# Optimization experiments

Measured on AMD Instinct MI355X. Metric: run time of the kernel, lower is better.

The kernel has to match this reference:

```python
import jax, jax.numpy as jnp
import numpy as np

B, S, D_MODEL, D_K, D_V = 8, 2048, 1024, 512, 512


def setup_inputs() -> dict:
    key = jax.random.key(0)
    ks = jax.random.split(key, 7)
    sq = jax.random.normal(ks[0], (B, S, D_MODEL), dtype=jnp.float32)
    skv = jax.random.normal(ks[1], (B, S, D_MODEL), dtype=jnp.float32)
    q_pad = jax.random.uniform(ks[2], (B, S)) < 0.1
    kv_pad = jax.random.uniform(ks[3], (B, S)) < 0.1
    Wq = jax.random.normal(ks[4], (D_MODEL, D_K), dtype=jnp.float32) * (D_MODEL ** -0.5)
    Wk = jax.random.normal(ks[5], (D_MODEL, D_K), dtype=jnp.float32) * (D_MODEL ** -0.5)
    Wv = jax.random.normal(ks[6], (D_MODEL, D_V), dtype=jnp.float32) * (D_MODEL ** -0.5)
    return {
        "source_query": sq,
        "source_key_value": skv,
        "source_query_padding_mask": q_pad,
        "source_key_value_padding_mask": kv_pad,
        "Wq": Wq,
        "Wk": Wk,
        "Wv": Wv,
    }


def reference(source_query, source_key_value, source_query_padding_mask,
              source_key_value_padding_mask, Wq, Wk, Wv):
    neg_inf = jnp.float32(-jnp.inf)
    q = source_query @ Wq          # [B,Sq,d_k]
    k = source_key_value @ Wk      # [B,Sk,d_k]
    v = source_key_value @ Wv      # [B,Sk,d_v]
    scale = jnp.float32(D_K) ** -0.5
    scores = jnp.einsum("bqd,bkd->bqk", q, k) * scale  # [B,Sq,Sk]
    # query padding mask broadcast along key dim, kv padding mask along query dim
    pad = source_query_padding_mask[:, :, None] | source_key_value_padding_mask[:, None, :]
    scores = jnp.where(pad, neg_inf, scores)
    # causal mask (masked=True): positions above diagonal blocked
    Sq = scores.shape[1]
    causal = jnp.tril(jnp.ones((Sq, Sq), dtype=bool))
    scores = jnp.where(causal[None, :, :], scores, neg_inf)
    attn = jax.nn.softmax(scores, axis=-1)
    # fully-masked rows produce NaN -> zero (matches torch nan masked_fill)
    attn = jnp.where(jnp.isnan(attn), jnp.float32(0.0), attn)
    # dropout p=0.0 (eval): identity
    out = jnp.einsum("bqk,bkv->bqv", attn, v)  # [B,Sq,d_v]
    return out
```

## Files before the change

kernel.cpp:

```cpp
#include <hip/hip_runtime.h>

typedef unsigned short u16;
typedef unsigned int   u32;
typedef __attribute__((ext_vector_type(4))) float  f32x4;
typedef __attribute__((ext_vector_type(8))) __bf16 bf16x8;

#define BATCH 8
#define SEQ   2048
#define DMODEL 1024
#define DK    512
#define DV    512
#define SCALE 0.044194173824159216f

__device__ __forceinline__ u16 f2bf(float f) {
  u32 u = __float_as_uint(f);
  return (u16)((u + 0x7fffu + ((u >> 16) & 1u)) >> 16);
}

__device__ __forceinline__ bool read_mask(const void* p, int idx, int mode) {
  if (mode == 1) return ((const unsigned char*)p)[idx] != 0;
  if (mode == 2) return ((const float*)p)[idx] != 0.0f;
  return ((const int*)p)[idx] != 0;
}

__device__ __forceinline__ void gl_lds16(const u16* g, u16* l) {
  __builtin_amdgcn_global_load_lds(
      (const __attribute__((address_space(1))) u32*)g,
      (__attribute__((address_space(3))) u32*)l, 16, 0, 0);
}

__global__ void detect_mode(const int* __restrict__ qp, int* __restrict__ flag) {
  __shared__ int f;
  if (threadIdx.x == 0) f = 0;
  __syncthreads();
  int local = 0;
  for (int i = threadIdx.x; i < 4096; i += 256) {
    int v = qp[i];
    if (v == 0x3F800000) local |= 2;
    else if (v != 0 && v != 1 && v != -1) local |= 1;
  }
  if (local) atomicOr(&f, local);
  __syncthreads();
  if (threadIdx.x == 0) {
    int m = 0;
    if (f & 2) m = 2; else if (f & 1) m = 1;
    *flag = m;
  }
}

__global__ __launch_bounds__(256) void wt_transpose(const float* __restrict__ W0,
                                                    const float* __restrict__ W1,
                                                    const float* __restrict__ W2,
                                                    u16* __restrict__ dst) {
  const float* W = (blockIdx.z == 0) ? W0 : (blockIdx.z == 1) ? W1 : W2;
  u16* out = dst + (size_t)blockIdx.z * (DK * DMODEL);
  __shared__ float T[32][33];
  int k0 = blockIdx.x * 32, n0 = blockIdx.y * 32;
  int tx = threadIdx.x, ty = threadIdx.y;
#pragma unroll
  for (int i = 0; i < 4; ++i) {
    int r = ty + i * 8;
    T[r][tx] = W[(size_t)(k0 + r) * DK + n0 + tx];
  }
  __syncthreads();
#pragma unroll
  for (int i = 0; i < 4; ++i) {
    int r = ty + i * 8;
    out[(size_t)(n0 + r) * DMODEL + k0 + tx] = f2bf(T[tx][r]);
  }
}

__global__ __launch_bounds__(256) void convert_bf16(const float* __restrict__ src,
                                                    u16* __restrict__ dst) {
  int i = (blockIdx.x * 256 + threadIdx.x) * 8;
  f32x4 a = *(const f32x4*)(src + i);
  f32x4 b = *(const f32x4*)(src + i + 4);
  uint4 o;
  o.x = (u32)f2bf(a[0]) | ((u32)f2bf(a[1]) << 16);
  o.y = (u32)f2bf(a[2]) | ((u32)f2bf(a[3]) << 16);
  o.z = (u32)f2bf(b[0]) | ((u32)f2bf(b[1]) << 16);
  o.w = (u32)f2bf(b[2]) | ((u32)f2bf(b[3]) << 16);
  *(uint4*)(dst + i) = o;
}

__global__ __launch_bounds__(256, 3) void proj_gemm(const u16* __restrict__ A,
                                                    const u16* __restrict__ Wt_base,
                                                    int z0, u16* __restrict__ dst0,
                                                    u16* __restrict__ dst1) {
  int z = z0 + blockIdx.z;
  const u16* Wt = Wt_base + (size_t)z * (DK * DMODEL);
  u16* dst = (z == 2) ? dst1 : dst0;
  int n0 = blockIdx.x * 128, m0 = blockIdx.y * 128;

  __shared__ __align__(16) u16 As[128 * 64];
  __shared__ __align__(16) u16 Bs[128 * 64];

  int tid = threadIdx.x, lane = tid & 63, w = tid >> 6;
  int wm = w & 1, wn = w >> 1;
  int l15 = lane & 15, lg = lane >> 4;
  int r3 = lane >> 3, c7 = lane & 7;
  int csw = c7 ^ r3;

  f32x4 acc[4][4];
#pragma unroll
  for (int m = 0; m < 4; ++m)
#pragma unroll
    for (int n = 0; n < 4; ++n) acc[m][n] = (f32x4)0.0f;

  for (int k0 = 0; k0 < DMODEL; k0 += 64) {
    __syncthreads();
#pragma unroll
    for (int u = 0; u < 4; ++u) {
      int t = w * 4 + u;
      gl_lds16(A  + (size_t)(m0 + t * 8 + r3) * DMODEL + k0 + csw * 8, &As[t * 512]);
      gl_lds16(Wt + (size_t)(n0 + t * 8 + r3) * DMODEL + k0 + csw * 8, &Bs[t * 512]);
    }
    __syncthreads();
#pragma unroll
    for (int ks = 0; ks < 2; ++ks) {
      bf16x8 af[4], bfv[4];
#pragma unroll
      for (int m = 0; m < 4; ++m) {
        int row = wm * 64 + m * 16 + l15;
        af[m] = *(const bf16x8*)&As[row * 64 + (((ks * 4 + lg) ^ (l15 & 7)) * 8)];
      }
#pragma unroll
      for (int n = 0; n < 4; ++n) {
        int row = wn * 64 + n * 16 + l15;
        bfv[n] = *(const bf16x8*)&Bs[row * 64 + (((ks * 4 + lg) ^ (l15 & 7)) * 8)];
      }
#pragma unroll
      for (int m = 0; m < 4; ++m)
#pragma unroll
        for (int n = 0; n < 4; ++n)
          acc[m][n] = __builtin_amdgcn_mfma_f32_16x16x32_bf16(af[m], bfv[n], acc[m][n], 0, 0, 0);
    }
  }

  if (z != 2) {
#pragma unroll
    for (int m = 0; m < 4; ++m) {
      int rowb = m0 + wm * 64 + m * 16;
#pragma unroll
      for (int n = 0; n < 4; ++n) {
        int col = n0 + wn * 64 + n * 16 + l15;
        size_t base = (size_t)(rowb >> 4) * 8192 + (size_t)(col >> 5) * 512 + (col & 31);
#pragma unroll
        for (int r = 0; r < 4; ++r)
          dst[base + (lg * 4 + r) * 32] = f2bf(acc[m][n][r]);
      }
    }
  } else {
#pragma unroll
    for (int m = 0; m < 4; ++m) {
      int row0 = m0 + wm * 64 + m * 16 + lg * 4;
      int b = row0 >> 11, s0 = row0 & 2047;
#pragma unroll
      for (int n = 0; n < 4; ++n) {
        int dv = n0 + wn * 64 + n * 16 + l15;
        size_t off = (size_t)b * (SEQ * DV) + (size_t)(dv >> 4) * 32768 +
                     (size_t)(s0 >> 5) * 512 + (dv & 15) * 32 + (s0 & 31);
        u16 tmp[4] __attribute__((aligned(8)));
#pragma unroll
        for (int r = 0; r < 4; ++r) tmp[r] = f2bf(acc[m][n][r]);
        *(uint2*)&dst[off] = *(const uint2*)tmp;
      }
    }
  }
}

__global__ __launch_bounds__(256, 2) void attn_kernel(
    const u16* __restrict__ Qf, const u16* __restrict__ Kf,
    const u16* __restrict__ Vf, const void* __restrict__ qpad,
    const void* __restrict__ kvpad, const int* __restrict__ flag,
    float* __restrict__ out) {
  __shared__ __align__(16) u16 Pbuf[32 * 72];
  __shared__ float partm[32 * 2];
  __shared__ float ald[32];
  __shared__ float partl[32 * 2];

  int tid = threadIdx.x;
  int lane = tid & 63, w = tid >> 6;
  int l15 = lane & 15, lg = lane >> 4;
  int wk = w & 1;
  int m  = w >> 1;
  int bi = blockIdx.x;
  int j = bi & 63, b = bi >> 6;
  int qt = (j & 1) ? (63 - (j >> 1)) : (j >> 1);
  int q0 = qt * 32;
  int mode = *flag;
  int lanoff = l15 * 32 + lg * 8;

  const u16* Qb = Qf + (size_t)b * (SEQ * DK);
  const u16* Kb = Kf + (size_t)b * (SEQ * DK);
  const u16* Vb = Vf + (size_t)b * (SEQ * DV);

  bf16x8 qf[16];
  {
    const u16* qp = Qb + (size_t)(qt * 2 + m) * 8192 + lanoff;
#pragma unroll
    for (int ks = 0; ks < 16; ++ks) qf[ks] = *(const bf16x8*)(qp + ks * 512);
  }

  f32x4 o[2][8];
#pragma unroll
  for (int m2 = 0; m2 < 2; ++m2)
#pragma unroll
    for (int n = 0; n < 8; ++n) o[m2][n] = (f32x4)0.0f;

  float mo[4], lsum[4];
#pragma unroll
  for (int r = 0; r < 4; ++r) { mo[r] = -1e38f; lsum[r] = 0.0f; }

  int nkt = (q0 + 95) >> 6;

  for (int kt = 0; kt < nkt; ++kt) {
    int k0 = kt * 64;

    f32x4 s0 = (f32x4)0.0f, s1 = (f32x4)0.0f;
    {
      const u16* kp0 = Kb + (size_t)((k0 >> 4) + wk * 2) * 8192 + lanoff;
      const u16* kp1 = kp0 + 8192;
#pragma unroll
      for (int ks = 0; ks < 16; ++ks) {
        bf16x8 b0 = *(const bf16x8*)(kp0 + ks * 512);
        bf16x8 b1 = *(const bf16x8*)(kp1 + ks * 512);
        s0 = __builtin_amdgcn_mfma_f32_16x16x32_bf16(qf[ks], b0, s0, 0, 0, 0);
        s1 = __builtin_amdgcn_mfma_f32_16x16x32_bf16(qf[ks], b1, s1, 0, 0, 0);
      }
    }

    float sv[2][4];
#pragma unroll
    for (int kg = 0; kg < 2; ++kg) {
      int key = k0 + wk * 32 + kg * 16 + l15;
      bool kvm = read_mask(kvpad, b * SEQ + key, mode);
#pragma unroll
      for (int r = 0; r < 4; ++r) {
        int qrow = q0 + m * 16 + lg * 4 + r;
        float x = (kg == 0 ? s0[r] : s1[r]) * SCALE;
        sv[kg][r] = (kvm || key > qrow) ? -__builtin_inff() : x;
      }
    }

    float wmax[4];
#pragma unroll
    for (int r = 0; r < 4; ++r) wmax[r] = fmaxf(sv[0][r], sv[1][r]);
#pragma unroll
    for (int d = 1; d < 16; d <<= 1)
#pragma unroll
      for (int r = 0; r < 4; ++r) wmax[r] = fmaxf(wmax[r], __shfl_xor(wmax[r], d));
    if (l15 == 0) {
#pragma unroll
      for (int r = 0; r < 4; ++r) partm[(m * 16 + lg * 4 + r) * 2 + wk] = wmax[r];
    }
    __syncthreads();

    float al[4], ws[4];
#pragma unroll
    for (int r = 0; r < 4; ++r) {
      int row = m * 16 + lg * 4 + r;
      float tm = fmaxf(partm[row * 2], partm[row * 2 + 1]);
      float mn = fmaxf(mo[r], fmaxf(tm, -1e38f));
      al[r] = __expf(mo[r] - mn);
      mo[r] = mn;
      float p0 = __expf(sv[0][r] - mn);
      float p1 = __expf(sv[1][r] - mn);
      Pbuf[row * 72 + wk * 32 + l15] = f2bf(p0);
      Pbuf[row * 72 + wk * 32 + 16 + l15] = f2bf(p1);
      ws[r] = p0 + p1;
    }
#pragma unroll
    for (int d = 1; d < 16; d <<= 1)
#pragma unroll
      for (int r = 0; r < 4; ++r) ws[r] += __shfl_xor(ws[r], d);
#pragma unroll
    for (int r = 0; r < 4; ++r) lsum[r] = lsum[r] * al[r] + ws[r];
    if (wk == 0 && l15 == 0) {
#pragma unroll
      for (int r = 0; r < 4; ++r) ald[m * 16 + lg * 4 + r] = al[r];
    }
    __syncthreads();

    float ar[2][4];
#pragma unroll
    for (int m2 = 0; m2 < 2; ++m2)
#pragma unroll
      for (int r = 0; r < 4; ++r) ar[m2][r] = ald[m2 * 16 + lg * 4 + r];
#pragma unroll
    for (int m2 = 0; m2 < 2; ++m2)
#pragma unroll
      for (int n = 0; n < 8; ++n)
#pragma unroll
        for (int r = 0; r < 4; ++r) o[m2][n][r] *= ar[m2][r];

    {
      const u16* vpb = Vb + (size_t)(w * 8) * 32768 + (size_t)(k0 >> 5) * 512 + lanoff;
#pragma unroll
      for (int ks = 0; ks < 2; ++ks) {
        bf16x8 pa0 = *(const bf16x8*)&Pbuf[(l15) * 72 + ks * 32 + lg * 8];
        bf16x8 pa1 = *(const bf16x8*)&Pbuf[(16 + l15) * 72 + ks * 32 + lg * 8];
#pragma unroll
        for (int n = 0; n < 4; ++n) {
          bf16x8 bv0 = *(const bf16x8*)(vpb + (size_t)(n * 2) * 32768 + ks * 512);
          bf16x8 bv1 = *(const bf16x8*)(vpb + (size_t)(n * 2 + 1) * 32768 + ks * 512);
          o[0][n * 2]     = __builtin_amdgcn_mfma_f32_16x16x32_bf16(pa0, bv0, o[0][n * 2], 0, 0, 0);
          o[1][n * 2]     = __builtin_amdgcn_mfma_f32_16x16x32_bf16(pa1, bv0, o[1][n * 2], 0, 0, 0);
          o[0][n * 2 + 1] = __builtin_amdgcn_mfma_f32_16x16x32_bf16(pa0, bv1, o[0][n * 2 + 1], 0, 0, 0);
          o[1][n * 2 + 1] = __builtin_amdgcn_mfma_f32_16x16x32_bf16(pa1, bv1, o[1][n * 2 + 1], 0, 0, 0);
        }
      }
    }
  }

  if (l15 == 0) {
#pragma unroll
    for (int r = 0; r < 4; ++r) partl[(m * 16 + lg * 4 + r) * 2 + wk] = lsum[r];
  }
  __syncthreads();
  {
    float f[2][4];
#pragma unroll
    for (int m2 = 0; m2 < 2; ++m2)
#pragma unroll
      for (int r = 0; r < 4; ++r) {
        int row = m2 * 16 + lg * 4 + r;
        float l = partl[row * 2] + partl[row * 2 + 1];
        bool qp = read_mask(qpad, b * SEQ + q0 + row, mode);
        f[m2][r] = (l > 0.0f && !qp) ? 1.0f / l : 0.0f;
      }
#pragma unroll
    for (int m2 = 0; m2 < 2; ++m2)
#pragma unroll
      for (int n = 0; n < 8; ++n) {
        int dv = w * 128 + n * 16 + l15;
#pragma unroll
        for (int r = 0; r < 4; ++r) {
          int row = m2 * 16 + lg * 4 + r;
          out[(size_t)(b * SEQ + q0 + row) * DV + dv] = o[m2][n][r] * f[m2][r];
        }
      }
  }
}

extern "C" void kernel_launch(void* const* d_in, const int* in_sizes, int n_in,
                              void* d_out, int out_size, void* d_ws, size_t ws_size,
                              hipStream_t stream) {
  const float* sq  = (const float*)d_in[0];
  const float* skv = (const float*)d_in[1];
  const void* qp   = d_in[2];
  const void* kvp  = d_in[3];
  const float* Wq  = (const float*)d_in[4];
  const float* Wk  = (const float*)d_in[5];
  const float* Wv  = (const float*)d_in[6];
  char* ws = (char*)d_ws;

  u16* Abf = (u16*)ws;
  u16* Qf  = (u16*)(ws + 33554432);
  u16* Kf  = (u16*)(ws + 50331648);
  u16* Vf  = (u16*)(ws + 67108864);
  u16* Wt  = (u16*)(ws + 83886080);
  int* flag = (int*)(ws + 87031808);

  wt_transpose<<<dim3(32, 16, 3), dim3(32, 8, 1), 0, stream>>>(Wq, Wk, Wv, Wt);
  detect_mode<<<1, 256, 0, stream>>>((const int*)qp, flag);

  convert_bf16<<<8192, 256, 0, stream>>>(sq, Abf);
  proj_gemm<<<dim3(4, 128, 1), dim3(256), 0, stream>>>(Abf, Wt, 0, Qf, Qf);

  convert_bf16<<<8192, 256, 0, stream>>>(skv, Abf);
  proj_gemm<<<dim3(4, 128, 2), dim3(256), 0, stream>>>(Abf, Wt, 1, Kf, Vf);

  attn_kernel<<<dim3(512), dim3(256), 0, stream>>>(Qf, Kf, Vf, qp, kvp, flag,
                                                   (float*)d_out);
}
```

Baseline: 471.9 us.

## Enlarge attention tiles to 64 queries by 128 keys with Q staged in LDS

After: 592.6 us. +25.6%, slower.

```diff
diff --git a/kernel.cpp b/kernel.cpp
--- a/kernel.cpp
+++ b/kernel.cpp
@@ -169,25 +169,24 @@
   }
 }
 
-__global__ __launch_bounds__(256, 2) void attn_kernel(
+#define KTILE 128
+#define PSTRIDE 136
+__global__ __launch_bounds__(256, 1) void attn_kernel(
     const u16* __restrict__ Qf, const u16* __restrict__ Kf,
     const u16* __restrict__ Vf, const void* __restrict__ qpad,
     const void* __restrict__ kvpad, const int* __restrict__ flag,
     float* __restrict__ out) {
-  __shared__ __align__(16) u16 Pbuf[32 * 72];
-  __shared__ float partm[32 * 2];
-  __shared__ float ald[32];
-  __shared__ float partl[32 * 2];
+  __shared__ __align__(16) u16 Qs[2 * 8192];
+  __shared__ __align__(16) u16 Pbuf[64 * PSTRIDE];
+  __shared__ __align__(16) float partm[64 * 4];
+  __shared__ __align__(16) float partl[64 * 4];
 
   int tid = threadIdx.x;
   int lane = tid & 63, w = tid >> 6;
   int l15 = lane & 15, lg = lane >> 4;
-  int wk = w & 1;
-  int m  = w >> 1;
   int bi = blockIdx.x;
-  int j = bi & 63, b = bi >> 6;
-  int qt = (j & 1) ? (63 - (j >> 1)) : (j >> 1);
-  int q0 = qt * 32;
+  int b = bi & 7, qt = bi >> 3;
+  int q0 = qt * 64;
   int mode = *flag;
   int lanoff = l15 * 32 + lg * 8;
 
@@ -195,149 +194,179 @@
   const u16* Kb = Kf + (size_t)b * (SEQ * DK);
   const u16* Vb = Vf + (size_t)b * (SEQ * DV);
 
-  bf16x8 qf[16];
-  {
-    const u16* qp = Qb + (size_t)(qt * 2 + m) * 8192 + lanoff;
-#pragma unroll
-    for (int ks = 0; ks < 16; ++ks) qf[ks] = *(const bf16x8*)(qp + ks * 512);
-  }
-
-  f32x4 o[2][8];
-#pragma unroll
-  for (int m2 = 0; m2 < 2; ++m2)
-#pragma unroll
-    for (int n = 0; n < 8; ++n) o[m2][n] = (f32x4)0.0f;
-
-  float mo[4], lsum[4];
-#pragma unroll
-  for (int r = 0; r < 4; ++r) { mo[r] = -1e38f; lsum[r] = 0.0f; }
-
-  int nkt = (q0 + 95) >> 6;
+#pragma unroll
+  for (int i = 0; i < 8; ++i) {
+    int t = w * 8 + i;
+    gl_lds16(Qb + (size_t)(qt * 4 + (t >> 4)) * 8192 + (size_t)(t & 15) * 512 + lane * 8,
+             &Qs[t * 512]);
+  }
+  bf16x8 qreg[2][16];
+#pragma unroll
+  for (int mm = 0; mm < 2; ++mm) {
+    const u16* qp = Qb + (size_t)(qt * 4 + 2 + mm) * 8192 + lanoff;
+#pragma unroll
+    for (int ks = 0; ks < 16; ++ks) qreg[mm][ks] = *(const bf16x8*)(qp + ks * 512);
+  }
+  __syncthreads();
+
+  f32x4 o[4][8];
+#pragma unroll
+  for (int m = 0; m < 4; ++m)
+#pragma unroll
+    for (int g = 0; g < 8; ++g) o[m][g] = (f32x4)0.0f;
+
+  float mo[4][4], lsum[4][4];
+#pragma unroll
+  for (int m = 0; m < 4; ++m)
+#pragma unroll
+    for (int r = 0; r < 4; ++r) { mo[m][r] = -1e38f; lsum[m][r] = 0.0f; }
+
+  int nkt = (q0 + 191) >> 7;
 
   for (int kt = 0; kt < nkt; ++kt) {
-    int k0 = kt * 64;
-
-    f32x4 s0 = (f32x4)0.0f, s1 = (f32x4)0.0f;
+    int k0 = kt * KTILE;
+    int kg0 = (k0 >> 4) + w * 2;
+
+    f32x4 s[4][2];
+#pragma unroll
+    for (int m = 0; m < 4; ++m) { s[m][0] = (f32x4)0.0f; s[m][1] = (f32x4)0.0f; }
     {
-      const u16* kp0 = Kb + (size_t)((k0 >> 4) + wk * 2) * 8192 + lanoff;
+      const u16* kp0 = Kb + (size_t)kg0 * 8192 + lanoff;
       const u16* kp1 = kp0 + 8192;
 #pragma unroll
       for (int ks = 0; ks < 16; ++ks) {
-        bf16x8 b0 = *(const bf16x8*)(kp0 + ks * 512);
-        bf16x8 b1 = *(const bf16x8*)(kp1 + ks * 512);
-        s0 = __builtin_amdgcn_mfma_f32_16x16x32_bf16(qf[ks], b0, s0, 0, 0, 0);
-        s1 = __builtin_amdgcn_mfma_f32_16x16x32_bf16(qf[ks], b1, s1, 0, 0, 0);
-      }
-    }
-
-    float sv[2][4];
-#pragma unroll
-    for (int kg = 0; kg < 2; ++kg) {
-      int key = k0 + wk * 32 + kg * 16 + l15;
-      bool kvm = read_mask(kvpad, b * SEQ + key, mode);
+        bf16x8 bk0 = *(const bf16x8*)(kp0 + ks * 512);
+        bf16x8 bk1 = *(const bf16x8*)(kp1 + ks * 512);
+        bf16x8 a0 = *(const bf16x8*)&Qs[ks * 512 + lanoff];
+        bf16x8 a1 = *(const bf16x8*)&Qs[8192 + ks * 512 + lanoff];
+        s[0][0] = __builtin_amdgcn_mfma_f32_16x16x32_bf16(a0, bk0, s[0][0], 0, 0, 0);
+        s[0][1] = __builtin_amdgcn_mfma_f32_16x16x32_bf16(a0, bk1, s[0][1], 0, 0, 0);
+        s[1][0] = __builtin_amdgcn_mfma_f32_16x16x32_bf16(a1, bk0, s[1][0], 0, 0, 0);
+        s[1][1] = __builtin_amdgcn_mfma_f32_16x16x32_bf16(a1, bk1, s[1][1], 0, 0, 0);
+        s[2][0] = __builtin_amdgcn_mfma_f32_16x16x32_bf16(qreg[0][ks], bk0, s[2][0], 0, 0, 0);
+        s[2][1] = __builtin_amdgcn_mfma_f32_16x16x32_bf16(qreg[0][ks], bk1, s[2][1], 0, 0, 0);
+        s[3][0] = __builtin_amdgcn_mfma_f32_16x16x32_bf16(qreg[1][ks], bk0, s[3][0], 0, 0, 0);
+        s[3][1] = __builtin_amdgcn_mfma_f32_16x16x32_bf16(qreg[1][ks], bk1, s[3][1], 0, 0, 0);
+      }
+    }
+
+    int key0 = k0 + w * 32 + l15;
+    bool kvm0 = read_mask(kvpad, b * SEQ + key0, mode);
+    bool kvm1 = read_mask(kvpad, b * SEQ + key0 + 16, mode);
+    float sv[4][2][4];
+#pragma unroll
+    for (int m = 0; m < 4; ++m)
 #pragma unroll
       for (int r = 0; r < 4; ++r) {
         int qrow = q0 + m * 16 + lg * 4 + r;
-        float x = (kg == 0 ? s0[r] : s1[r]) * SCALE;
-        sv[kg][r] = (kvm || key > qrow) ? -__builtin_inff() : x;
-      }
-    }
-
-    float wmax[4];
-#pragma unroll
-    for (int r = 0; r < 4; ++r) wmax[r] = fmaxf(sv[0][r], sv[1][r]);
+        float x0 = s[m][0][r] * SCALE;
+        float x1 = s[m][1][r] * SCALE;
+        sv[m][0][r] = (kvm0 || key0 > qrow) ? -__builtin_inff() : x0;
+        sv[m][1][r] = (kvm1 || key0 + 16 > qrow) ? -__builtin_inff() : x1;
+      }
+
+    float wmax[4][4];
+#pragma unroll
+    for (int m = 0; m < 4; ++m)
+#pragma unroll
+      for (int r = 0; r < 4; ++r) wmax[m][r] = fmaxf(sv[m][0][r], sv[m][1][r]);
 #pragma unroll
     for (int d = 1; d < 16; d <<= 1)
 #pragma unroll
-      for (int r = 0; r < 4; ++r) wmax[r] = fmaxf(wmax[r], __shfl_xor(wmax[r], d));
+      for (int m = 0; m < 4; ++m)
+#pragma unroll
+        for (int r = 0; r < 4; ++r)
+          wmax[m][r] = fmaxf(wmax[m][r], __shfl_xor(wmax[m][r], d));
     if (l15 == 0) {
 #pragma unroll
-      for (int r = 0; r < 4; ++r) partm[(m * 16 + lg * 4 + r) * 2 + wk] = wmax[r];
+      for (int m = 0; m < 4; ++m)
+#pragma unroll
+        for (int r = 0; r < 4; ++r) partm[(m * 16 + lg * 4 + r) * 4 + w] = wmax[m][r];
     }
     __syncthreads();
 
-    float al[4], ws[4];
-#pragma unroll
-    for (int r = 0; r < 4; ++r) {
-      int row = m * 16 + lg * 4 + r;
-      float tm = fmaxf(partm[row * 2], partm[row * 2 + 1]);
-      float mn = fmaxf(mo[r], fmaxf(tm, -1e38f));
-      al[r] = __expf(mo[r] - mn);
-      mo[r] = mn;
-      float p0 = __expf(sv[0][r] - mn);
-      float p1 = __expf(sv[1][r] - mn);
-      Pbuf[row * 72 + wk * 32 + l15] = f2bf(p0);
-      Pbuf[row * 72 + wk * 32 + 16 + l15] = f2bf(p1);
-      ws[r] = p0 + p1;
-    }
+    float al[4][4], ws[4][4];
+#pragma unroll
+    for (int m = 0; m < 4; ++m)
+#pragma unroll
+      for (int r = 0; r < 4; ++r) {
+        int row = m * 16 + lg * 4 + r;
+        f32x4 pm = *(const f32x4*)&partm[row * 4];
+        float tm = fmaxf(fmaxf(pm[0], pm[1]), fmaxf(pm[2], pm[3]));
+        float mn = fmaxf(mo[m][r], fmaxf(tm, -1e38f));
+        al[m][r] = __expf(mo[m][r] - mn);
+        mo[m][r] = mn;
+        float p0 = __expf(sv[m][0][r] - mn);
+        float p1 = __expf(sv[m][1][r] - mn);
+        Pbuf[row * PSTRIDE + w * 32 + l15] = f2bf(p0);
+        Pbuf[row * PSTRIDE + w * 32 + 16 + l15] = f2bf(p1);
+        ws[m][r] = p0 + p1;
+      }
 #pragma unroll
     for (int d = 1; d < 16; d <<= 1)
 #pragma unroll
-      for (int r = 0; r < 4; ++r) ws[r] += __shfl_xor(ws[r], d);
-#pragma unroll
-    for (int r = 0; r < 4; ++r) lsum[r] = lsum[r] * al[r] + ws[r];
-    if (wk == 0 && l15 == 0) {
-#pragma unroll
-      for (int r = 0; r < 4; ++r) ald[m * 16 + lg * 4 + r] = al[r];
-    }
+      for (int m = 0; m < 4; ++m)
+#pragma unroll
+        for (int r = 0; r < 4; ++r) ws[m][r] += __shfl_xor(ws[m][r], d);
+#pragma unroll
+    for (int m = 0; m < 4; ++m)
+#pragma unroll
+      for (int r = 0; r < 4; ++r) lsum[m][r] = lsum[m][r] * al[m][r] + ws[m][r];
+
+#pragma unroll
+    for (int m = 0; m < 4; ++m)
+#pragma unroll
+      for (int g = 0; g < 8; ++g)
+#pragma unroll
+        for (int r = 0; r < 4; ++r) o[m][g][r] *= al[m][r];
+
     __syncthreads();
 
-    float ar[2][4];
-#pragma unroll
-    for (int m2 = 0; m2 < 2; ++m2)
-#pragma unroll
-      for (int r = 0; r < 4; ++r) ar[m2][r] = ald[m2 * 16 + lg * 4 + r];
-#pragma unroll
-    for (int m2 = 0; m2 < 2; ++m2)
-#pragma unroll
-      for (int n = 0; n < 8; ++n)
-#pragma unroll
-        for (int r = 0; r < 4; ++r) o[m2][n][r] *= ar[m2][r];
-
-    {
-      const u16* vpb = Vb + (size_t)(w * 8) * 32768 + (size_t)(k0 >> 5) * 512 + lanoff;
-#pragma unroll
-      for (int ks = 0; ks < 2; ++ks) {
-        bf16x8 pa0 = *(const bf16x8*)&Pbuf[(l15) * 72 + ks * 32 + lg * 8];
-        bf16x8 pa1 = *(const bf16x8*)&Pbuf[(16 + l15) * 72 + ks * 32 + lg * 8];
-#pragma unroll
-        for (int n = 0; n < 4; ++n) {
-          bf16x8 bv0 = *(const bf16x8*)(vpb + (size_t)(n * 2) * 32768 + ks * 512);
-          bf16x8 bv1 = *(const bf16x8*)(vpb + (size_t)(n * 2 + 1) * 32768 + ks * 512);
-          o[0][n * 2]     = __builtin_amdgcn_mfma_f32_16x16x32_bf16(pa0, bv0, o[0][n * 2], 0, 0, 0);
-          o[1][n * 2]     = __builtin_amdgcn_mfma_f32_16x16x32_bf16(pa1, bv0, o[1][n * 2], 0, 0, 0);
-          o[0][n * 2 + 1] = __builtin_amdgcn_mfma_f32_16x16x32_bf16(pa0, bv1, o[0][n * 2 + 1], 0, 0, 0);
-          o[1][n * 2 + 1] = __builtin_amdgcn_mfma_f32_16x16x32_bf16(pa1, bv1, o[1][n * 2 + 1], 0, 0, 0);
-        }
+#pragma unroll
+    for (int ks2 = 0; ks2 < 4; ++ks2) {
+      bf16x8 pa[4];
+#pragma unroll
+      for (int m = 0; m < 4; ++m)
+        pa[m] = *(const bf16x8*)&Pbuf[(m * 16 + l15) * PSTRIDE + ks2 * 32 + lg * 8];
+      const u16* vp = Vb + (size_t)(w * 8) * 32768 + (size_t)(kt * 4 + ks2) * 512 + lanoff;
+#pragma unroll
+      for (int g = 0; g < 8; ++g) {
+        bf16x8 bv = *(const bf16x8*)(vp + (size_t)g * 32768);
+#pragma unroll
+        for (int m = 0; m < 4; ++m)
+          o[m][g] = __builtin_amdgcn_mfma_f32_16x16x32_bf16(pa[m], bv, o[m][g], 0, 0, 0);
       }
     }
   }
 
   if (l15 == 0) {
 #pragma unroll
-    for (int r = 0; r < 4; ++r) partl[(m * 16 + lg * 4 + r) * 2 + wk] = lsum[r];
+    for (int m = 0; m < 4; ++m)
+#pragma unroll
+      for (int r = 0; r < 4; ++r) partl[(m * 16 + lg * 4 + r) * 4 + w] = lsum[m][r];
   }
   __syncthreads();
   {
-    float f[2][4];
-#pragma unroll
-    for (int m2 = 0; m2 < 2; ++m2)
+    float f[4][4];
+#pragma unroll
+    for (int m = 0; m < 4; ++m)
 #pragma unroll
       for (int r = 0; r < 4; ++r) {
-        int row = m2 * 16 + lg * 4 + r;
-        float l = partl[row * 2] + partl[row * 2 + 1];
+        int row = m * 16 + lg * 4 + r;
+        f32x4 pl = *(const f32x4*)&partl[row * 4];
+        float l = pl[0] + pl[1] + pl[2] + pl[3];
         bool qp = read_mask(qpad, b * SEQ + q0 + row, mode);
-        f[m2][r] = (l > 0.0f && !qp) ? 1.0f / l : 0.0f;
-      }
-#pragma unroll
-    for (int m2 = 0; m2 < 2; ++m2)
-#pragma unroll
-      for (int n = 0; n < 8; ++n) {
-        int dv = w * 128 + n * 16 + l15;
+        f[m][r] = (l > 0.0f && !qp) ? 1.0f / l : 0.0f;
+      }
+#pragma unroll
+    for (int m = 0; m < 4; ++m)
+#pragma unroll
+      for (int g = 0; g < 8; ++g) {
+        int dv = w * 128 + g * 16 + l15;
 #pragma unroll
         for (int r = 0; r < 4; ++r) {
-          int row = m2 * 16 + lg * 4 + r;
-          out[(size_t)(b * SEQ + q0 + row) * DV + dv] = o[m2][n][r] * f[m2][r];
+          int row = m * 16 + lg * 4 + r;
+          out[(size_t)(b * SEQ + q0 + row) * DV + dv] = o[m][g][r] * f[m][r];
         }
       }
   }
@@ -371,6 +400,6 @@
   convert_bf16<<<8192, 256, 0, stream>>>(skv, Abf);
   proj_gemm<<<dim3(4, 128, 2), dim3(256), 0, stream>>>(Abf, Wt, 1, Kf, Vf);
 
-  attn_kernel<<<dim3(512), dim3(256), 0, stream>>>(Qf, Kf, Vf, qp, kvp, flag,
+  attn_kernel<<<dim3(256), dim3(256), 0, stream>>>(Qf, Kf, Vf, qp, kvp, flag,
                                                    (float*)d_out);
 }
```

## Restructure attention into 16-row tiles with register-resident softmax, no LDS or barriers

Applied to the files above, without the earlier changes.

Result: slower. 706.3 us (+49.7%).

```diff
diff --git a/kernel.cpp b/kernel.cpp
--- a/kernel.cpp
+++ b/kernel.cpp
@@ -159,7 +159,7 @@
       for (int n = 0; n < 4; ++n) {
         int dv = n0 + wn * 64 + n * 16 + l15;
         size_t off = (size_t)b * (SEQ * DV) + (size_t)(dv >> 4) * 32768 +
-                     (size_t)(s0 >> 5) * 512 + (dv & 15) * 32 + (s0 & 31);
+                     (size_t)(s0 >> 5) * 512 + (dv & 15) * 32 + lg * 8 + (m & 1) * 4;
         u16 tmp[4] __attribute__((aligned(8)));
 #pragma unroll
         for (int r = 0; r < 4; ++r) tmp[r] = f2bf(acc[m][n][r]);
@@ -169,177 +169,125 @@
   }
 }
 
-__global__ __launch_bounds__(256, 2) void attn_kernel(
+__global__ __launch_bounds__(128, 2) void attn_kernel(
     const u16* __restrict__ Qf, const u16* __restrict__ Kf,
     const u16* __restrict__ Vf, const void* __restrict__ qpad,
     const void* __restrict__ kvpad, const int* __restrict__ flag,
     float* __restrict__ out) {
-  __shared__ __align__(16) u16 Pbuf[32 * 72];
-  __shared__ float partm[32 * 2];
-  __shared__ float ald[32];
-  __shared__ float partl[32 * 2];
-
   int tid = threadIdx.x;
-  int lane = tid & 63, w = tid >> 6;
+  int lane = tid & 63;
+  int dvh = tid >> 6;
   int l15 = lane & 15, lg = lane >> 4;
-  int wk = w & 1;
-  int m  = w >> 1;
   int bi = blockIdx.x;
-  int j = bi & 63, b = bi >> 6;
-  int qt = (j & 1) ? (63 - (j >> 1)) : (j >> 1);
-  int q0 = qt * 32;
+  int b = bi & 7;
+  int qt = 127 - (bi >> 3);
+  int q0 = qt * 16;
   int mode = *flag;
   int lanoff = l15 * 32 + lg * 8;
+  int q = q0 + l15;
 
   const u16* Qb = Qf + (size_t)b * (SEQ * DK);
   const u16* Kb = Kf + (size_t)b * (SEQ * DK);
-  const u16* Vb = Vf + (size_t)b * (SEQ * DV);
+  const u16* Vb = Vf + (size_t)b * (SEQ * DV) + (size_t)(dvh * 16) * 32768;
 
   bf16x8 qf[16];
   {
-    const u16* qp = Qb + (size_t)(qt * 2 + m) * 8192 + lanoff;
+    const u16* qp = Qb + (size_t)qt * 8192 + lanoff;
 #pragma unroll
     for (int ks = 0; ks < 16; ++ks) qf[ks] = *(const bf16x8*)(qp + ks * 512);
   }
 
-  f32x4 o[2][8];
-#pragma unroll
-  for (int m2 = 0; m2 < 2; ++m2)
-#pragma unroll
-    for (int n = 0; n < 8; ++n) o[m2][n] = (f32x4)0.0f;
-
-  float mo[4], lsum[4];
-#pragma unroll
-  for (int r = 0; r < 4; ++r) { mo[r] = -1e38f; lsum[r] = 0.0f; }
-
-  int nkt = (q0 + 95) >> 6;
+  f32x4 o[16];
+#pragma unroll
+  for (int g = 0; g < 16; ++g) o[g] = (f32x4)0.0f;
+
+  float mo = -1e38f, lsum = 0.0f;
+  int nkt = (q0 + 47) >> 5;
 
   for (int kt = 0; kt < nkt; ++kt) {
-    int k0 = kt * 64;
+    int k0 = kt * 32;
 
     f32x4 s0 = (f32x4)0.0f, s1 = (f32x4)0.0f;
     {
-      const u16* kp0 = Kb + (size_t)((k0 >> 4) + wk * 2) * 8192 + lanoff;
-      const u16* kp1 = kp0 + 8192;
+      const u16* kp = Kb + (size_t)(k0 >> 4) * 8192 + lanoff;
 #pragma unroll
       for (int ks = 0; ks < 16; ++ks) {
-        bf16x8 b0 = *(const bf16x8*)(kp0 + ks * 512);
-        bf16x8 b1 = *(const bf16x8*)(kp1 + ks * 512);
-        s0 = __builtin_amdgcn_mfma_f32_16x16x32_bf16(qf[ks], b0, s0, 0, 0, 0);
-        s1 = __builtin_amdgcn_mfma_f32_16x16x32_bf16(qf[ks], b1, s1, 0, 0, 0);
-      }
-    }
-
-    float sv[2][4];
-#pragma unroll
-    for (int kg = 0; kg < 2; ++kg) {
-      int key = k0 + wk * 32 + kg * 16 + l15;
-      bool kvm = read_mask(kvpad, b * SEQ + key, mode);
+        bf16x8 a0 = *(const bf16x8*)(kp + ks * 512);
+        bf16x8 a1 = *(const bf16x8*)(kp + 8192 + ks * 512);
+        s0 = __builtin_amdgcn_mfma_f32_16x16x32_bf16(a0, qf[ks], s0, 0, 0, 0);
+        s1 = __builtin_amdgcn_mfma_f32_16x16x32_bf16(a1, qf[ks], s1, 0, 0, 0);
+      }
+    }
+
+    float sv0[4], sv1[4];
+#pragma unroll
+    for (int r = 0; r < 4; ++r) {
+      int key0 = k0 + lg * 4 + r;
+      bool msk0 = read_mask(kvpad, b * SEQ + key0, mode) || (key0 > q);
+      bool msk1 = read_mask(kvpad, b * SEQ + key0 + 16, mode) || (key0 + 16 > q);
+      sv0[r] = msk0 ? -__builtin_inff() : s0[r] * SCALE;
+      sv1[r] = msk1 ? -__builtin_inff() : s1[r] * SCALE;
+    }
+
+    float tmax = fmaxf(fmaxf(fmaxf(sv0[0], sv0[1]), fmaxf(sv0[2], sv0[3])),
+                       fmaxf(fmaxf(sv1[0], sv1[1]), fmaxf(sv1[2], sv1[3])));
+    tmax = fmaxf(tmax, __shfl_xor(tmax, 16));
+    tmax = fmaxf(tmax, __shfl_xor(tmax, 32));
+
+    float mn = fmaxf(mo, fmaxf(tmax, -1e38f));
+    float al = __expf(mo - mn);
+    mo = mn;
+
+    float p0[4], p1[4];
+    float psum = 0.0f;
+#pragma unroll
+    for (int r = 0; r < 4; ++r) {
+      p0[r] = __expf(sv0[r] - mn);
+      p1[r] = __expf(sv1[r] - mn);
+      psum += p0[r] + p1[r];
+    }
+    psum += __shfl_xor(psum, 16);
+    psum += __shfl_xor(psum, 32);
+    lsum = lsum * al + psum;
+
+    u16 pk[8] __attribute__((aligned(16)));
+#pragma unroll
+    for (int r = 0; r < 4; ++r) { pk[r] = f2bf(p0[r]); pk[4 + r] = f2bf(p1[r]); }
+    bf16x8 pa = *(const bf16x8*)pk;
+
+    float alr[4];
+#pragma unroll
+    for (int r = 0; r < 4; ++r) alr[r] = __shfl(al, lg * 4 + r);
+#pragma unroll
+    for (int g = 0; g < 16; ++g)
+#pragma unroll
+      for (int r = 0; r < 4; ++r) o[g][r] *= alr[r];
+
+    {
+      const u16* vp = Vb + (size_t)kt * 512 + lanoff;
+#pragma unroll
+      for (int g = 0; g < 16; ++g) {
+        bf16x8 bv = *(const bf16x8*)(vp + (size_t)g * 32768);
+        o[g] = __builtin_amdgcn_mfma_f32_16x16x32_bf16(pa, bv, o[g], 0, 0, 0);
+      }
+    }
+  }
+
+  {
+    bool qpm = read_mask(qpad, b * SEQ + q, mode);
+    float linv = (lsum > 0.0f && !qpm) ? 1.0f / lsum : 0.0f;
+    float lr[4];
+#pragma unroll
+    for (int r = 0; r < 4; ++r) lr[r] = __shfl(linv, lg * 4 + r);
+#pragma unroll
+    for (int g = 0; g < 16; ++g) {
+      int dv = dvh * 256 + g * 16 + l15;
 #pragma unroll
       for (int r = 0; r < 4; ++r) {
-        int qrow = q0 + m * 16 + lg * 4 + r;
-        float x = (kg == 0 ? s0[r] : s1[r]) * SCALE;
-        sv[kg][r] = (kvm || key > qrow) ? -__builtin_inff() : x;
-      }
-    }
-
-    float wmax[4];
-#pragma unroll
-    for (int r = 0; r < 4; ++r) wmax[r] = fmaxf(sv[0][r], sv[1][r]);
-#pragma unroll
-    for (int d = 1; d < 16; d <<= 1)
-#pragma unroll
-      for (int r = 0; r < 4; ++r) wmax[r] = fmaxf(wmax[r], __shfl_xor(wmax[r], d));
-    if (l15 == 0) {
-#pragma unroll
-      for (int r = 0; r < 4; ++r) partm[(m * 16 + lg * 4 + r) * 2 + wk] = wmax[r];
-    }
-    __syncthreads();
-
-    float al[4], ws[4];
-#pragma unroll
-    for (int r = 0; r < 4; ++r) {
-      int row = m * 16 + lg * 4 + r;
-      float tm = fmaxf(partm[row * 2], partm[row * 2 + 1]);
-      float mn = fmaxf(mo[r], fmaxf(tm, -1e38f));
-      al[r] = __expf(mo[r] - mn);
-      mo[r] = mn;
-      float p0 = __expf(sv[0][r] - mn);
-      float p1 = __expf(sv[1][r] - mn);
-      Pbuf[row * 72 + wk * 32 + l15] = f2bf(p0);
-      Pbuf[row * 72 + wk * 32 + 16 + l15] = f2bf(p1);
-      ws[r] = p0 + p1;
-    }
-#pragma unroll
-    for (int d = 1; d < 16; d <<= 1)
-#pragma unroll
-      for (int r = 0; r < 4; ++r) ws[r] += __shfl_xor(ws[r], d);
-#pragma unroll
-    for (int r = 0; r < 4; ++r) lsum[r] = lsum[r] * al[r] + ws[r];
-    if (wk == 0 && l15 == 0) {
-#pragma unroll
-      for (int r = 0; r < 4; ++r) ald[m * 16 + lg * 4 + r] = al[r];
-    }
-    __syncthreads();
-
-    float ar[2][4];
-#pragma unroll
-    for (int m2 = 0; m2 < 2; ++m2)
-#pragma unroll
-      for (int r = 0; r < 4; ++r) ar[m2][r] = ald[m2 * 16 + lg * 4 + r];
-#pragma unroll
-    for (int m2 = 0; m2 < 2; ++m2)
-#pragma unroll
-      for (int n = 0; n < 8; ++n)
-#pragma unroll
-        for (int r = 0; r < 4; ++r) o[m2][n][r] *= ar[m2][r];
-
-    {
-      const u16* vpb = Vb + (size_t)(w * 8) * 32768 + (size_t)(k0 >> 5) * 512 + lanoff;
-#pragma unroll
-      for (int ks = 0; ks < 2; ++ks) {
-        bf16x8 pa0 = *(const bf16x8*)&Pbuf[(l15) * 72 + ks * 32 + lg * 8];
-        bf16x8 pa1 = *(const bf16x8*)&Pbuf[(16 + l15) * 72 + ks * 32 + lg * 8];
-#pragma unroll
-        for (int n = 0; n < 4; ++n) {
-          bf16x8 bv0 = *(const bf16x8*)(vpb + (size_t)(n * 2) * 32768 + ks * 512);
-          bf16x8 bv1 = *(const bf16x8*)(vpb + (size_t)(n * 2 + 1) * 32768 + ks * 512);
-          o[0][n * 2]     = __builtin_amdgcn_mfma_f32_16x16x32_bf16(pa0, bv0, o[0][n * 2], 0, 0, 0);
-          o[1][n * 2]     = __builtin_amdgcn_mfma_f32_16x16x32_bf16(pa1, bv0, o[1][n * 2], 0, 0, 0);
-          o[0][n * 2 + 1] = __builtin_amdgcn_mfma_f32_16x16x32_bf16(pa0, bv1, o[0][n * 2 + 1], 0, 0, 0);
-          o[1][n * 2 + 1] = __builtin_amdgcn_mfma_f32_16x16x32_bf16(pa1, bv1, o[1][n * 2 + 1], 0, 0, 0);
-        }
-      }
-    }
-  }
-
-  if (l15 == 0) {
-#pragma unroll
-    for (int r = 0; r < 4; ++r) partl[(m * 16 + lg * 4 + r) * 2 + wk] = lsum[r];
-  }
-  __syncthreads();
-  {
-    float f[2][4];
-#pragma unroll
-    for (int m2 = 0; m2 < 2; ++m2)
-#pragma unroll
-      for (int r = 0; r < 4; ++r) {
-        int row = m2 * 16 + lg * 4 + r;
-        float l = partl[row * 2] + partl[row * 2 + 1];
-        bool qp = read_mask(qpad, b * SEQ + q0 + row, mode);
-        f[m2][r] = (l > 0.0f && !qp) ? 1.0f / l : 0.0f;
-      }
-#pragma unroll
-    for (int m2 = 0; m2 < 2; ++m2)
-#pragma unroll
-      for (int n = 0; n < 8; ++n) {
-        int dv = w * 128 + n * 16 + l15;
-#pragma unroll
-        for (int r = 0; r < 4; ++r) {
-          int row = m2 * 16 + lg * 4 + r;
-          out[(size_t)(b * SEQ + q0 + row) * DV + dv] = o[m2][n][r] * f[m2][r];
-        }
-      }
+        int row = q0 + lg * 4 + r;
+        out[(size_t)(b * SEQ + row) * DV + dv] = o[g][r] * lr[r];
+      }
+    }
   }
 }
 
@@ -371,6 +319,6 @@
   convert_bf16<<<8192, 256, 0, stream>>>(skv, Abf);
   proj_gemm<<<dim3(4, 128, 2), dim3(256), 0, stream>>>(Abf, Wt, 1, Kf, Vf);
 
-  attn_kernel<<<dim3(512), dim3(256), 0, stream>>>(Qf, Kf, Vf, qp, kvp, flag,
-                                                   (float*)d_out);
-}
+  attn_kernel<<<dim3(1024), dim3(128), 0, stream>>>(Qf, Kf, Vf, qp, kvp, flag,
+                                                    (float*)d_out);
+}
```
